# Kernel optimization log

Measured on AMD Instinct MI355X. Metric: run time of the kernel, lower is better.

The kernel has to match this reference:

```python
import jax, jax.numpy as jnp
import numpy as np

B, T, C = 2, 2048, 1024
H = 16
D = C // H          # 64
HID = C // 4        # meta_net bottleneck = 256
FF = 4 * C          # 4096


def setup_inputs() -> dict:
    key = jax.random.key(0)
    ks = jax.random.split(key, 11)
    s = lambda fan_in: 1.0 / np.sqrt(fan_in)
    inp = {
        "x": jax.random.normal(ks[0], (B, T, C), jnp.float32),
        # torch nn.Linear weights are [out, in]
        "Wq": jax.random.uniform(ks[1], (C, C), jnp.float32, -s(C), s(C)),
        "Wk": jax.random.uniform(ks[2], (C, C), jnp.float32, -s(C), s(C)),
        "Wv": jax.random.uniform(ks[3], (C, C), jnp.float32, -s(C), s(C)),
        "Wm1": jax.random.uniform(ks[4], (HID, C), jnp.float32, -s(C), s(C)),
        "bm1": jax.random.uniform(ks[5], (HID,), jnp.float32, -s(C), s(C)),
        "Wm2": jax.random.uniform(ks[6], (H, HID), jnp.float32, -s(HID), s(HID)),
        "bm2": jax.random.uniform(ks[7], (H,), jnp.float32, -s(HID), s(HID)),
        "Wproj": jax.random.uniform(ks[8], (C, C), jnp.float32, -s(C), s(C)),
        "Wfc": jax.random.uniform(ks[9], (FF, C), jnp.float32, -s(C), s(C)),
        "Wcp": jax.random.uniform(ks[10], (C, FF), jnp.float32, -s(FF), s(FF)),
    }
    return inp


def _rms_norm(x):
    eps = jnp.finfo(x.dtype).eps
    return x * jax.lax.rsqrt(jnp.mean(jnp.square(x), axis=-1, keepdims=True) + eps)


def reference(x, Wq, Wk, Wv, Wm1, bm1, Wm2, bm2, Wproj, Wfc, Wcp):
    b, t, c = x.shape
    h = Wm2.shape[0]
    d = c // h
    q = (x @ Wq.T).reshape(b, t, h, d)
    k = (x @ Wk.T).reshape(b, t, h, d)
    v = (x @ Wv.T).reshape(b, t, h, d)
    surprise = jax.nn.sigmoid(jnp.maximum(x @ Wm1.T + bm1, 0.0) @ Wm2.T + bm2)  # [b,t,h]
    decay = 1.0 - surprise

    # time-major for scan: [t, b, h, ...]
    qT = jnp.transpose(q, (1, 0, 2, 3))
    kT = jnp.transpose(k, (1, 0, 2, 3))
    vT = jnp.transpose(v, (1, 0, 2, 3))
    dT = jnp.transpose(decay, (1, 0, 2))     # [t,b,h]
    gT = jnp.transpose(surprise, (1, 0, 2))  # [t,b,h]

    def step(state, inp):
        qt, kt, vt, dt, gt = inp
        # state: [b,h,d,d]; decay-gated rank-1 update
        state = state * dt[..., None, None] + gt[..., None, None] * (kt[..., :, None] * vt[..., None, :])
        yt = jnp.einsum('bhd,bhde->bhe', qt, state)
        return state, yt

    state0 = jnp.zeros((b, h, d, d), x.dtype)
    _, ys = jax.lax.scan(step, state0, (qT, kT, vT, dT, gT))  # ys: [t,b,h,d]
    y = jnp.transpose(ys, (1, 0, 2, 3)).reshape(b, t, c)
    y = y @ Wproj.T
    yn = _rms_norm(y)
    mlp = jnp.square(jnp.maximum(yn @ Wfc.T, 0.0)) @ Wcp.T
    return y + mlp
```

## Files before the change

### kernel.cpp

```cpp
#include <hip/hip_runtime.h>
#include <math.h>

#define BB   2
#define TT   2048
#define CC   1024
#define HH   16
#define DD   64
#define HID  256
#define FFD  4096
#define NTOK (BB*TT)
#define CT   64
#define NC   (TT/CT)
#define NBH  (BB*HH)
#define NCHK (NBH*NC)
#define MB   (1048576ULL)

typedef unsigned short u16;
typedef unsigned int   u32;
typedef __attribute__((ext_vector_type(8))) short frag8;
typedef __attribute__((ext_vector_type(4))) float f32x4;

__device__ __forceinline__ float bf2f(u16 h){
    union { u32 u; float f; } c; c.u = ((u32)h) << 16; return c.f;
}
__device__ __forceinline__ u16 f2bf(float f){
    union { float f; u32 u; } c; c.f = f;
    u32 u = c.u;
    u += 0x7FFFu + ((u >> 16) & 1u);
    return (u16)(u >> 16);
}
__device__ __forceinline__ bool is_f32(const u32* flags, int idx) {
    if (idx == -2) return true;
    if (idx < 0)  return false;
    return flags[idx] != 0;
}

__device__ __forceinline__ void gload16(const void* g, void* l) {
    __builtin_amdgcn_global_load_lds(
        (const __attribute__((address_space(1))) u32*)g,
        (__attribute__((address_space(3))) u32*)l, 16, 0, 0);
}

struct InPtrs { const void* p[11]; int n[11]; };

__global__ __launch_bounds__(64)
void sniff_kernel(InPtrs ip, u32* __restrict__ flags)
{
    int lane = threadIdx.x;
    u32 f0 = 0;
    for (int i = 0; i < 11; i++) {
        const u16* p = (const u16*)ip.p[i];
        int cap = ip.n[i] < 256 ? ip.n[i] : 256;
        bool ok = true;
        for (int j = lane; j < cap; j += 64) {
            u16 u = p[j];
            u32 e = (u >> 7) & 0xFFu;
            bool good = (u == 0u) || (u == 0x8000u) || (e >= 64u && e < 192u);
            ok = ok && good;
        }
        unsigned long long ball = __ballot(ok);
        u32 fl = (ball == ~0ull) ? 0u : 1u;
        if (ip.n[i] < 64) fl = f0;
        if (i == 0) f0 = fl;
        if (lane == 0) flags[i] = fl;
    }
}

struct ConvArgs {
    const void* src[6];
    u16* dst[6];
    int flag[6];
    int bstart[7];
    int nseg;
};

__global__ __launch_bounds__(256)
void conv_kernel(ConvArgs a, const u32* __restrict__ flags)
{
    int b = blockIdx.x;
    int s = 0;
    #pragma unroll
    for (int i = 1; i < 6; i++) if (i < a.nseg && b >= a.bstart[i]) s = i;
    size_t off = ((size_t)(b - a.bstart[s])) * 2048 + (size_t)threadIdx.x * 8;
    u16* d = a.dst[s] + off;
    if (flags[a.flag[s]] != 0) {
        const float* sp = (const float*)a.src[s] + off;
        float4 x0 = *(const float4*)sp;
        float4 x1 = *(const float4*)(sp + 4);
        u16 buf[8];
        buf[0]=f2bf(x0.x); buf[1]=f2bf(x0.y); buf[2]=f2bf(x0.z); buf[3]=f2bf(x0.w);
        buf[4]=f2bf(x1.x); buf[5]=f2bf(x1.y); buf[6]=f2bf(x1.z); buf[7]=f2bf(x1.w);
        *(uint4*)d = *(uint4*)buf;
    } else {
        *(uint4*)d = *(const uint4*)((const u16*)a.src[s] + off);
    }
}

__device__ __forceinline__ void xcd_map(int i, int NB, int gx, int& bm, int& bn)
{
    int per = NB >> 3;
    int iq  = (i & 7) * per + (i >> 3);
    bm = iq / gx;
    bn = iq % gx;
}

template<int MODE, int BN>
__global__ __launch_bounds__(256)
void gemm_nt(const u16* __restrict__ A, const u16* __restrict__ B,
             void* Cm, void* Cm2, const void* aux,
             int M, int N, int K, int lda, int ldb,
             const u32* __restrict__ flags, int oi)
{
    constexpr int NFR = BN / 32;
    const bool of32 = is_f32(flags, oi);
    __shared__ u16 As[2][128 * 32];
    __shared__ u16 Bs[2][BN * 32];
    const int tid = threadIdx.x;
    int bm, bn;
    xcd_map(blockIdx.x, gridDim.x, N / BN, bm, bn);
    const int z = blockIdx.y;
    const size_t koff = (size_t)z * K;

    const int wave = tid >> 6, lane = tid & 63;
    const int lm = lane & 15, quad = lane >> 4;
    const int wm = (wave >> 1) * 64, wn = (wave & 1) * (BN / 2);

    const int srow = lane >> 2;
    const int scol = (lane & 3) * 8;
    const u16* gA = A + (size_t)(bm*128 + wave*32 + srow)*lda + koff + scol;
    const int brow = (BN == 128) ? (wave*32 + srow) : (wave*16 + srow);
    const u16* gB = B + (size_t)(bn*BN + brow)*ldb + koff + scol;
    const size_t a16 = (size_t)16 * lda, b16 = (size_t)16 * ldb;

    f32x4 acc[4][NFR];
    #pragma unroll
    for (int i = 0; i < 4; i++)
        #pragma unroll
        for (int j = 0; j < NFR; j++)
            acc[i][j] = (f32x4){0.f, 0.f, 0.f, 0.f};

    auto stage = [&](int buf, int kk) {
        gload16(gA + kk,       &As[buf][wave*1024]);
        gload16(gA + kk + a16, &As[buf][wave*1024 + 512]);
        if constexpr (BN == 128) {
            gload16(gB + kk,       &Bs[buf][wave*1024]);
            gload16(gB + kk + b16, &Bs[buf][wave*1024 + 512]);
        } else {
            gload16(gB + kk, &Bs[buf][wave*512]);
        }
    };

    stage(0, 0);
    __syncthreads();
    int cur = 0;
    for (int k0 = 0; k0 < K; k0 += 32) {
        if (k0 + 32 < K) stage(cur ^ 1, k0 + 32);
        frag8 af[4], bfr[NFR];
        #pragma unroll
        for (int i = 0; i < 4; i++)
            af[i]  = *(frag8*)&As[cur][(wm + i*16 + lm)*32 + quad*8];
        #pragma unroll
        for (int j = 0; j < NFR; j++)
            bfr[j] = *(frag8*)&Bs[cur][(wn + j*16 + lm)*32 + quad*8];
        #pragma unroll
        for (int i = 0; i < 4; i++)
            #pragma unroll
            for (int j = 0; j < NFR; j++)
                acc[i][j] = __builtin_amdgcn_mfma_f32_16x16x32_bf16(
                    af[i], bfr[j], acc[i][j], 0, 0, 0);
        __syncthreads();
        cur ^= 1;
    }

    float* outF = (float*)(z ? Cm2 : Cm);
    #pragma unroll
    for (int i = 0; i < 4; i++) {
        #pragma unroll
        for (int j = 0; j < NFR; j++) {
            const int gcol = bn*BN + wn + j*16 + lm;
            #pragma unroll
            for (int r = 0; r < 4; r++) {
                const int grow = bm*128 + wm + i*16 + quad*4 + r;
                size_t off = (size_t)grow * N + gcol;
                float vv = acc[i][j][r];
                if constexpr (MODE == 0) {
                    outF[off] = vv;
                } else if constexpr (MODE == 2) {
                    vv = fmaxf(vv, 0.f);
                    ((u16*)Cm)[off] = f2bf(vv * vv);
                } else {
                    float res = of32 ? ((const float*)aux)[off]
                                     : bf2f(((const u16*)aux)[off]);
                    vv += res;
                    if (of32) ((float*)Cm)[off] = vv;
                    else      ((u16*)Cm)[off]   = f2bf(vv);
                }
            }
        }
    }
}

__global__ __launch_bounds__(256)
void gemm_qkvm(const u16* __restrict__ xb,
               const u16* __restrict__ Wqb, const u16* __restrict__ Wkb,
               const u16* __restrict__ Wvb, const u16* __restrict__ Wm1b,
               const void* __restrict__ bm1,
               u16* __restrict__ q, u16* __restrict__ k, u16* __restrict__ v,
               float* __restrict__ hid, const u32* __restrict__ flags)
{
    __shared__ u16 As[2][128 * 32];
    __shared__ u16 Bs[2][128 * 32];
    const int tid = threadIdx.x;
    int bm, bn;
    xcd_map(blockIdx.x, 832, 26, bm, bn);

    const int bsel = bn >> 3;
    const u16* B = (bsel == 0) ? Wqb : (bsel == 1) ? Wkb
                 : (bsel == 2) ? Wvb : Wm1b;

    const int wave = tid >> 6, lane = tid & 63;
    const int lm = lane & 15, quad = lane >> 4;
    const int wm = (wave >> 1) * 64, wn = (wave & 1) * 64;

    const int srow = lane >> 2;
    const int scol = (lane & 3) * 8;
    const u16* gA = xb + (size_t)(bm*128 + wave*32 + srow)*CC + scol;
    const u16* gB = B + (size_t)((bn & 7)*128 + wave*32 + srow)*CC + scol;
    const size_t s16 = (size_t)16 * CC;

    f32x4 acc[4][4];
    #pragma unroll
    for (int i = 0; i < 4; i++)
        #pragma unroll
        for (int j = 0; j < 4; j++)
            acc[i][j] = (f32x4){0.f, 0.f, 0.f, 0.f};

    auto stage = [&](int buf, int kk) {
        gload16(gA + kk,       &As[buf][wave*1024]);
        gload16(gA + kk + s16, &As[buf][wave*1024 + 512]);
        gload16(gB + kk,       &Bs[buf][wave*1024]);
        gload16(gB + kk + s16, &Bs[buf][wave*1024 + 512]);
    };

    stage(0, 0);
    __syncthreads();
    int cur = 0;
    for (int k0 = 0; k0 < CC; k0 += 32) {
        if (k0 + 32 < CC) stage(cur ^ 1, k0 + 32);
        frag8 af[4], bfr[4];
        #pragma unroll
        for (int i = 0; i < 4; i++) {
            af[i]  = *(frag8*)&As[cur][(wm + i*16 + lm)*32 + quad*8];
            bfr[i] = *(frag8*)&Bs[cur][(wn + i*16 + lm)*32 + quad*8];
        }
        #pragma unroll
        for (int i = 0; i < 4; i++)
            #pragma unroll
            for (int j = 0; j < 4; j++)
                acc[i][j] = __builtin_amdgcn_mfma_f32_16x16x32_bf16(
                    af[i], bfr[j], acc[i][j], 0, 0, 0);
        __syncthreads();
        cur ^= 1;
    }

    if (bsel < 3) {
        u16* outp = (bsel == 0) ? q : (bsel == 1) ? k : v;
        #pragma unroll
        for (int i = 0; i < 4; i++) {
            #pragma unroll
            for (int j = 0; j < 4; j++) {
                const int gcol = (bn & 7)*128 + wn + j*16 + lm;
                #pragma unroll
                for (int r = 0; r < 4; r++) {
                    const int grow = bm*128 + wm + i*16 + quad*4 + r;
                    outp[(size_t)grow * CC + gcol] = f2bf(acc[i][j][r]);
                }
            }
        }
    } else {
        const bool biasf = is_f32(flags, 5);
        #pragma unroll
        for (int i = 0; i < 4; i++) {
            #pragma unroll
            for (int j = 0; j < 4; j++) {
                const int gcol = (bn & 7)*128 + wn + j*16 + lm;
                float bia = biasf ? ((const float*)bm1)[gcol]
                                  : bf2f(((const u16*)bm1)[gcol]);
                #pragma unroll
                for (int r = 0; r < 4; r++) {
                    const int grow = bm*128 + wm + i*16 + quad*4 + r;
                    hid[(size_t)grow * HID + gcol] = fmaxf(acc[i][j][r] + bia, 0.f);
                }
            }
        }
    }
}

__global__ __launch_bounds__(256)
void meta2_kernel(const float* __restrict__ hid, const void* __restrict__ Wm2,
                  const void* __restrict__ bm2, float* __restrict__ g,
                  float* __restrict__ dec, const u32* __restrict__ flags)
{
    const bool wf = is_f32(flags, 6);
    const bool bf = is_f32(flags, 7);
    __shared__ float hs[16][257];
    __shared__ float wsm[16][257];
    int tid  = threadIdx.x;
    int tok0 = blockIdx.x * 16;
    for (int i = tid; i < 16*256; i += 256) {
        wsm[i >> 8][i & 255] = wf ? ((const float*)Wm2)[i] : bf2f(((const u16*)Wm2)[i]);
        hs [i >> 8][i & 255] = hid[(size_t)tok0*256 + i];
    }
    __syncthreads();
    int tok = tid >> 4, hh = tid & 15;
    float s = 0.f;
    #pragma unroll 8
    for (int kk = 0; kk < 256; kk++) s = fmaf(hs[tok][kk], wsm[hh][kk], s);
    s += bf ? ((const float*)bm2)[hh] : bf2f(((const u16*)bm2)[hh]);
    float sg = 1.f / (1.f + expf(-s));
    int idx = (tok0 + tok) * HH + hh;
    g[idx]   = sg;
    dec[idx] = 1.f - sg;
}

__global__ __launch_bounds__(256)
void scan_pass1(const u16* __restrict__ kbuf, const u16* __restrict__ vbuf,
                const float* __restrict__ g, const float* __restrict__ dec,
                float* __restrict__ Mb, float* __restrict__ Pb)
{
    __shared__ float ks[64*64];
    __shared__ float vs[64*64];
    __shared__ float dd[64], gg[64], cum[64], sw[64];
    int tid = threadIdx.x;
    int bhc = blockIdx.x;
    int c = bhc & 31, h = (bhc >> 5) & 15, b = bhc >> 9;
    int t0 = c * CT;
    size_t rowbase = ((size_t)(b*TT + t0))*CC + h*DD;

    for (int i = tid; i < 4096; i += 256) {
        int s = i >> 6, d = i & 63;
        ks[i] = bf2f(kbuf[rowbase + (size_t)s*CC + d]);
        vs[i] = bf2f(vbuf[rowbase + (size_t)s*CC + d]);
    }
    if (tid < 64) {
        int gidx = (b*TT + t0 + tid)*HH + h;
        dd[tid] = dec[gidx];
        gg[tid] = g[gidx];
    }
    __syncthreads();
    if (tid == 0) {
        float cs = 0.f;
        for (int s = 0; s < 64; s++) { cs += logf(fmaxf(dd[s], 1e-30f)); cum[s] = cs; }
    }
    __syncthreads();
    float ctot = cum[63];
    if (tid < 64) sw[tid] = gg[tid] * expf(ctot - cum[tid]);
    __syncthreads();

    int d0 = (tid >> 4) * 4, e0 = (tid & 15) * 4;
    float m[4][4] = {};
    for (int s = 0; s < 64; s++) {
        float w = sw[s];
        float4 kv = *(const float4*)&ks[s*64 + d0];
        float4 vv = *(const float4*)&vs[s*64 + e0];
        float a0 = w*kv.x, a1 = w*kv.y, a2 = w*kv.z, a3 = w*kv.w;
        m[0][0]=fmaf(a0,vv.x,m[0][0]); m[0][1]=fmaf(a0,vv.y,m[0][1]); m[0][2]=fmaf(a0,vv.z,m[0][2]); m[0][3]=fmaf(a0,vv.w,m[0][3]);
        m[1][0]=fmaf(a1,vv.x,m[1][0]); m[1][1]=fmaf(a1,vv.y,m[1][1]); m[1][2]=fmaf(a1,vv.z,m[1][2]); m[1][3]=fmaf(a1,vv.w,m[1][3]);
        m[2][0]=fmaf(a2,vv.x,m[2][0]); m[2][1]=fmaf(a2,vv.y,m[2][1]); m[2][2]=fmaf(a2,vv.z,m[2][2]); m[2][3]=fmaf(a2,vv.w,m[2][3]);
        m[3][0]=fmaf(a3,vv.x,m[3][0]); m[3][1]=fmaf(a3,vv.y,m[3][1]); m[3][2]=fmaf(a3,vv.z,m[3][2]); m[3][3]=fmaf(a3,vv.w,m[3][3]);
    }
    size_t base = (size_t)bhc * 4096;
    #pragma unroll
    for (int i = 0; i < 4; i++) {
        float4 o = make_float4(m[i][0], m[i][1], m[i][2], m[i][3]);
        *(float4*)&Mb[base + (size_t)(d0 + i)*64 + e0] = o;
    }
    if (tid == 0) Pb[bhc] = expf(ctot);
}

__global__ __launch_bounds__(256)
void scan_pass2(float* __restrict__ MS, const float* __restrict__ Pb)
{
    int bh = blockIdx.x, tid = threadIdx.x;
    float st[16];
    #pragma unroll
    for (int i = 0; i < 16; i++) st[i] = 0.f;
    for (int c = 0; c < NC; c++) {
        size_t base = ((size_t)bh*NC + c) * 4096;
        float p = Pb[bh*NC + c];
        #pragma unroll
        for (int i = 0; i < 16; i++) {
            size_t e = base + tid + i*256;
            float m = MS[e];
            MS[e] = st[i];
            st[i] = fmaf(p, st[i], m);
        }
    }
}

__global__ __launch_bounds__(256)
void scan_pass3(const u16* __restrict__ qbuf, const u16* __restrict__ kbuf,
                const u16* __restrict__ vbuf, const float* __restrict__ g,
                const float* __restrict__ dec, const float* __restrict__ Sb,
                u16* __restrict__ y)
{
    __shared__ float qs[64*64];
    __shared__ float kt[64*68];
    __shared__ float vs[64*64];
    __shared__ u16   Aws[4096];
    __shared__ float dd[64], gg[64], cum[64];
    int tid = threadIdx.x;
    int bhc = blockIdx.x;
    int c = bhc & 31, h = (bhc >> 5) & 15, b = bhc >> 9;
    int t0 = c * CT;
    size_t rowbase = ((size_t)(b*TT + t0))*CC + h*DD;

    for (int i = tid; i < 4096; i += 256) {
        int s = i >> 6, d = i & 63;
        size_t gi = rowbase + (size_t)s*CC + d;
        qs[i]        = bf2f(qbuf[gi]);
        kt[d*68 + s] = bf2f(kbuf[gi]);
        vs[i]        = bf2f(vbuf[gi]);
    }
    if (tid < 64) {
        int gidx = (b*TT + t0 + tid)*HH + h;
        dd[tid] = dec[gidx];
        gg[tid] = g[gidx];
    }
    __syncthreads();
    if (tid == 0) {
        float cs = 0.f;
        for (int s = 0; s < 64; s++) { cs += logf(fmaxf(dd[s], 1e-30f)); cum[s] = cs; }
    }
    __syncthreads();

    const int tt0 = (tid >> 4) * 4, ss0 = (tid & 15) * 4;
    float a1[4][4] = {};
    for (int d = 0; d < 64; d++) {
        float4 kv = *(const float4*)&kt[d*68 + ss0];
        #pragma unroll
        for (int i = 0; i < 4; i++) {
            float qv = qs[(tt0 + i)*64 + d];
            a1[i][0] = fmaf(qv, kv.x, a1[i][0]);
            a1[i][1] = fmaf(qv, kv.y, a1[i][1]);
            a1[i][2] = fmaf(qv, kv.z, a1[i][2]);
            a1[i][3] = fmaf(qv, kv.w, a1[i][3]);
        }
    }
    #pragma unroll
    for (int i = 0; i < 4; i++) {
        int t = tt0 + i;
        float ct = cum[t];
        #pragma unroll
        for (int j = 0; j < 4; j++) {
            int s = ss0 + j;
            float w = (s <= t) ? gg[s] * expf(ct - cum[s]) : 0.f;
            Aws[t*64 + s] = f2bf(w * a1[i][j]);
        }
    }
    __syncthreads();
    float* Ss = kt;
    size_t sbase = (size_t)bhc * 4096;
    for (int i = tid; i < 4096; i += 256) Ss[i] = Sb[sbase + i];
    __syncthreads();

    const int e0 = ss0;
    float o1[4][4] = {}, o2[4][4] = {};
    for (int s = 0; s < 64; s++) {
        float4 vv = *(const float4*)&vs[s*64 + e0];
        #pragma unroll
        for (int i = 0; i < 4; i++) {
            float av = bf2f(Aws[(tt0 + i)*64 + s]);
            o1[i][0] = fmaf(av, vv.x, o1[i][0]);
            o1[i][1] = fmaf(av, vv.y, o1[i][1]);
            o1[i][2] = fmaf(av, vv.z, o1[i][2]);
            o1[i][3] = fmaf(av, vv.w, o1[i][3]);
        }
    }
    for (int d = 0; d < 64; d++) {
        float4 sv = *(const float4*)&Ss[d*64 + e0];
        #pragma unroll
        for (int i = 0; i < 4; i++) {
            float qv = qs[(tt0 + i)*64 + d];
            o2[i][0] = fmaf(qv, sv.x, o2[i][0]);
            o2[i][1] = fmaf(qv, sv.y, o2[i][1]);
            o2[i][2] = fmaf(qv, sv.z, o2[i][2]);
            o2[i][3] = fmaf(qv, sv.w, o2[i][3]);
        }
    }
    #pragma unroll
    for (int i = 0; i < 4; i++) {
        float cd = expf(cum[tt0 + i]);
        size_t obase = rowbase + (size_t)(tt0 + i)*CC + e0;
        #pragma unroll
        for (int j = 0; j < 4; j++)
            y[obase + j] = f2bf(fmaf(cd, o2[i][j], o1[i][j]));
    }
}

__global__ __launch_bounds__(256)
void rmsnorm_kernel(const float* __restrict__ p0, const float* __restrict__ p1,
                    void* __restrict__ yres, u16* __restrict__ yn,
                    const u32* __restrict__ flags)
{
    const bool of32 = flags[0] != 0;
    __shared__ float red[4];
    __shared__ float sscale;
    int row = blockIdx.x, tid = threadIdx.x;
    size_t base = (size_t)row*CC + tid*4;
    float4 a = *(const float4*)&p0[base];
    float4 b = *(const float4*)&p1[base];
    float v0 = a.x + b.x, v1 = a.y + b.y, v2 = a.z + b.z, v3 = a.w + b.w;
    if (of32) {
        *(float4*)((float*)yres + base) = make_float4(v0, v1, v2, v3);
    } else {
        u16* yr = (u16*)yres + base;
        yr[0] = f2bf(v0); yr[1] = f2bf(v1); yr[2] = f2bf(v2); yr[3] = f2bf(v3);
    }
    float p = v0*v0 + v1*v1 + v2*v2 + v3*v3;
    #pragma unroll
    for (int off = 32; off > 0; off >>= 1) p += __shfl_down(p, off, 64);
    if ((tid & 63) == 0) red[tid >> 6] = p;
    __syncthreads();
    if (tid == 0) {
        float tot = red[0] + red[1] + red[2] + red[3];
        sscale = rsqrtf(tot * (1.0f/1024.0f) + 1.1920928955078125e-07f);
    }
    __syncthreads();
    float sc = sscale;
    yn[base + 0] = f2bf(v0 * sc);
    yn[base + 1] = f2bf(v1 * sc);
    yn[base + 2] = f2bf(v2 * sc);
    yn[base + 3] = f2bf(v3 * sc);
}

extern "C" void kernel_launch(void* const* d_in, const int* in_sizes, int n_in,
                              void* d_out, int out_size, void* d_ws, size_t ws_size,
                              hipStream_t stream)
{
    char* ws = (char*)d_ws;
    u16*   xb     = (u16*)  (ws + 32*MB);
    u16*   Wqb    = (u16*)  (ws + 40*MB);
    u16*   Wkb    = (u16*)  (ws + 42*MB);
    u16*   Wvb    = (u16*)  (ws + 44*MB);
    u16*   Wm1b   = (u16*)  (ws + 46*MB);
    u16*   Wprojb = (u16*)  (ws + 8*MB);
    u16*   q      = (u16*)  (ws + 0*MB);
    u16*   k      = (u16*)  (ws + 16*MB);
    u16*   v      = (u16*)  (ws + 24*MB);
    float* hid    = (float*)(ws + 10*MB);
    float* g      = (float*)(ws + 14*MB);
    float* dec    = (float*)(ws + 14*MB + 262144);
    float* Pb     = (float*)(ws + 14*MB + 524288);
    float* MS     = (float*)(ws + 32*MB);
    u16*   yat    = q;
    float* p0     = (float*)(ws + 16*MB);
    float* p1     = (float*)(ws + 32*MB);
    u16*   yn     = (u16*)  (ws + 0*MB);
    u16*   Wfcb   = (u16*)  (ws + 8*MB);
    u16*   h1     = (u16*)  (ws + 16*MB);
    u16*   Wcpb   = (u16*)  (ws + 0*MB);
    u32*   flags  = (u32*)  (ws + 48*MB);

    InPtrs ip;
    for (int i = 0; i < 11; i++) { ip.p[i] = d_in[i]; ip.n[i] = in_sizes[i]; }
    sniff_kernel<<<1, 64, 0, stream>>>(ip, flags);

    ConvArgs c1{};
    c1.src[0] = d_in[0]; c1.dst[0] = xb;     c1.flag[0] = 0;
    c1.src[1] = d_in[1]; c1.dst[1] = Wqb;    c1.flag[1] = 1;
    c1.src[2] = d_in[2]; c1.dst[2] = Wkb;    c1.flag[2] = 2;
    c1.src[3] = d_in[3]; c1.dst[3] = Wvb;    c1.flag[3] = 3;
    c1.src[4] = d_in[4]; c1.dst[4] = Wm1b;   c1.flag[4] = 4;
    c1.src[5] = d_in[8]; c1.dst[5] = Wprojb; c1.flag[5] = 8;
    {
        int nb[6] = {2048, 512, 512, 512, 128, 512};
        int cum = 0;
        for (int i = 0; i < 6; i++) { c1.bstart[i] = cum; cum += nb[i]; }
        c1.bstart[6] = cum;
        c1.nseg = 6;
        conv_kernel<<<cum, 256, 0, stream>>>(c1, flags);
    }

    gemm_qkvm<<<832, 256, 0, stream>>>(xb, Wqb, Wkb, Wvb, Wm1b, d_in[5],
                                       q, k, v, hid, flags);
    meta2_kernel<<<NTOK/16, 256, 0, stream>>>(hid, d_in[6], d_in[7], g, dec, flags);
    scan_pass1<<<NCHK, 256, 0, stream>>>(k, v, g, dec, MS, Pb);
    scan_pass2<<<NBH, 256, 0, stream>>>(MS, Pb);
    scan_pass3<<<NCHK, 256, 0, stream>>>(q, k, v, g, dec, MS, yat);
    gemm_nt<0,128><<<dim3(256, 2), 256, 0, stream>>>(yat, Wprojb, p0, p1, nullptr,
        NTOK, CC, 512, CC, CC, flags, -2);
    ConvArgs c2{};
    c2.src[0] = d_in[9]; c2.dst[0] = Wfcb; c2.flag[0] = 9;
    c2.bstart[0] = 0; for (int i = 1; i < 7; i++) c2.bstart[i] = 2048;
    c2.nseg = 1;
    conv_kernel<<<2048, 256, 0, stream>>>(c2, flags);
    rmsnorm_kernel<<<NTOK, 256, 0, stream>>>(p0, p1, d_out, yn, flags);
    gemm_nt<2,128><<<dim3(1024, 1), 256, 0, stream>>>(yn, Wfcb, h1, nullptr, nullptr,
        NTOK, FFD, CC, CC, CC, flags, -1);
    ConvArgs c3{};
    c3.src[0] = d_in[10]; c3.dst[0] = Wcpb; c3.flag[0] = 10;
    c3.bstart[0] = 0; for (int i = 1; i < 7; i++) c3.bstart[i] = 2048;
    c3.nseg = 1;
    conv_kernel<<<2048, 256, 0, stream>>>(c3, flags);
    gemm_nt<3,64><<<dim3(512, 1), 256, 0, stream>>>(h1, Wcpb, d_out, nullptr, d_out,
        NTOK, CC, FFD, FFD, FFD, flags, 0);
}
```

Baseline: 439.3 us.

## Triple-buffer GEMM LDS staging with explicit vmcnt waits; widen scan_pass2 grid

Both GEMM kernels move from double to triple LDS buffers, prefetching two k-tiles ahead. Each loop iteration now uses one raw barrier with a partial s_waitcnt vmcnt instead of two __syncthreads, to hide global-load latency and cut barrier overhead. scan_pass2 is split into 16 blocks per (b,h), each owning 256 state elements, so the serial chunk scan uses 512 blocks instead of 32. The extra LDS buffer lowers occupancy, and the hand-written waitcnt counts have to match the number of loads issued per stage.

```diff
diff --git a/kernel.cpp b/kernel.cpp
--- a/kernel.cpp
+++ b/kernel.cpp
@@ -41,6 +41,18 @@
         (__attribute__((address_space(3))) u32*)l, 16, 0, 0);
 }
 
+template<int N> __device__ __forceinline__ void wait_vm() {
+    if constexpr (N == 0)      asm volatile("s_waitcnt vmcnt(0)" ::: "memory");
+    else if constexpr (N == 3) asm volatile("s_waitcnt vmcnt(3)" ::: "memory");
+    else                       asm volatile("s_waitcnt vmcnt(4)" ::: "memory");
+}
+__device__ __forceinline__ void wait_lgkm0() {
+    asm volatile("s_waitcnt lgkmcnt(0)" ::: "memory");
+}
+__device__ __forceinline__ void barrier_raw() {
+    asm volatile("s_barrier" ::: "memory");
+}
+
 struct InPtrs { const void* p[11]; int n[11]; };
 
 __global__ __launch_bounds__(64)
@@ -112,9 +124,10 @@
              const u32* __restrict__ flags, int oi)
 {
     constexpr int NFR = BN / 32;
+    constexpr int NL  = (BN == 128) ? 4 : 3;
     const bool of32 = is_f32(flags, oi);
-    __shared__ u16 As[2][128 * 32];
-    __shared__ u16 Bs[2][BN * 32];
+    __shared__ u16 As[3][128 * 32];
+    __shared__ u16 Bs[3][BN * 32];
     const int tid = threadIdx.x;
     int bm, bn;
     xcd_map(blockIdx.x, gridDim.x, N / BN, bm, bn);
@@ -150,11 +163,18 @@
         }
     };
 
+    const int nt = K >> 5;
     stage(0, 0);
-    __syncthreads();
+    stage(1, 32);
     int cur = 0;
-    for (int k0 = 0; k0 < K; k0 += 32) {
-        if (k0 + 32 < K) stage(cur ^ 1, k0 + 32);
+    for (int t = 0; t < nt; ++t) {
+        if (t + 1 < nt) wait_vm<NL>();
+        else            wait_vm<0>();
+        barrier_raw();
+        if (t + 2 < nt) {
+            int fre = (cur >= 1) ? cur - 1 : cur + 2;
+            stage(fre, (t + 2) << 5);
+        }
         frag8 af[4], bfr[NFR];
         #pragma unroll
         for (int i = 0; i < 4; i++)
@@ -168,8 +188,8 @@
             for (int j = 0; j < NFR; j++)
                 acc[i][j] = __builtin_amdgcn_mfma_f32_16x16x32_bf16(
                     af[i], bfr[j], acc[i][j], 0, 0, 0);
-        __syncthreads();
-        cur ^= 1;
+        wait_lgkm0();
+        cur = (cur == 2) ? 0 : cur + 1;
     }
 
     float* outF = (float*)(z ? Cm2 : Cm);
@@ -208,8 +228,8 @@
                u16* __restrict__ q, u16* __restrict__ k, u16* __restrict__ v,
                float* __restrict__ hid, const u32* __restrict__ flags)
 {
-    __shared__ u16 As[2][128 * 32];
-    __shared__ u16 Bs[2][128 * 32];
+    __shared__ u16 As[3][128 * 32];
+    __shared__ u16 Bs[3][128 * 32];
     const int tid = threadIdx.x;
     int bm, bn;
     xcd_map(blockIdx.x, 832, 26, bm, bn);
@@ -242,11 +262,18 @@
         gload16(gB + kk + s16, &Bs[buf][wave*1024 + 512]);
     };
 
+    const int nt = CC >> 5;
     stage(0, 0);
-    __syncthreads();
+    stage(1, 32);
     int cur = 0;
-    for (int k0 = 0; k0 < CC; k0 += 32) {
-        if (k0 + 32 < CC) stage(cur ^ 1, k0 + 32);
+    for (int t = 0; t < nt; ++t) {
+        if (t + 1 < nt) wait_vm<4>();
+        else            wait_vm<0>();
+        barrier_raw();
+        if (t + 2 < nt) {
+            int fre = (cur >= 1) ? cur - 1 : cur + 2;
+            stage(fre, (t + 2) << 5);
+        }
         frag8 af[4], bfr[4];
         #pragma unroll
         for (int i = 0; i < 4; i++) {
@@ -259,8 +286,8 @@
             for (int j = 0; j < 4; j++)
                 acc[i][j] = __builtin_amdgcn_mfma_f32_16x16x32_bf16(
                     af[i], bfr[j], acc[i][j], 0, 0, 0);
-        __syncthreads();
-        cur ^= 1;
+        wait_lgkm0();
+        cur = (cur == 2) ? 0 : cur + 1;
     }
 
     if (bsel < 3) {
@@ -381,20 +408,15 @@
 __global__ __launch_bounds__(256)
 void scan_pass2(float* __restrict__ MS, const float* __restrict__ Pb)
 {
-    int bh = blockIdx.x, tid = threadIdx.x;
-    float st[16];
-    #pragma unroll
-    for (int i = 0; i < 16; i++) st[i] = 0.f;
+    int bh = blockIdx.x >> 4, grp = blockIdx.x & 15, tid = threadIdx.x;
+    int eo = grp*256 + tid;
+    float st = 0.f;
     for (int c = 0; c < NC; c++) {
-        size_t base = ((size_t)bh*NC + c) * 4096;
+        size_t e = ((size_t)bh*NC + c) * 4096 + eo;
         float p = Pb[bh*NC + c];
-        #pragma unroll
-        for (int i = 0; i < 16; i++) {
-            size_t e = base + tid + i*256;
-            float m = MS[e];
-            MS[e] = st[i];
-            st[i] = fmaf(p, st[i], m);
-        }
+        float m = MS[e];
+        MS[e] = st;
+        st = fmaf(p, st, m);
     }
 }
 
@@ -586,7 +608,7 @@
                                        q, k, v, hid, flags);
     meta2_kernel<<<NTOK/16, 256, 0, stream>>>(hid, d_in[6], d_in[7], g, dec, flags);
     scan_pass1<<<NCHK, 256, 0, stream>>>(k, v, g, dec, MS, Pb);
-    scan_pass2<<<NBH, 256, 0, stream>>>(MS, Pb);
+    scan_pass2<<<NBH*16, 256, 0, stream>>>(MS, Pb);
     scan_pass3<<<NCHK, 256, 0, stream>>>(q, k, v, g, dec, MS, yat);
     gemm_nt<0,128><<<dim3(256, 2), 256, 0, stream>>>(yat, Wprojb, p0, p1, nullptr,
         NTOK, CC, 512, CC, CC, flags, -2);
```

New measurement: 431.0 us. Within noise of the previous version (-1.9%).
